# Kernel tuning notes

Hardware: AMD Instinct MI355X
Metric: run time of the kernel (lower is better)

The kernel has to match this reference:

```python
import jax, jax.numpy as jnp
import numpy as np

N, C = 16384, 4096

def setup_inputs() -> dict:
    key = jax.random.key(0)
    k1, k2 = jax.random.split(key)
    preds = jax.random.normal(k1, (N, C), dtype=jnp.float32)
    targets = jax.random.normal(k2, (N, C), dtype=jnp.float32)
    return {"preds": preds, "targets": targets}


def reference(preds, targets):
    # Faithful to My_impute_Loss.forward: the module only RETURNS
    # clusters_pcc_loss + clusters_cossim_loss (per-column stats, axis=1 loop
    # / cosine_similarity(dim=0)); everything else in loss_function is unused.

    # --- per-column Pearson correlation over rows (vectorizes the axis=1 loop) ---
    mu_t = targets.mean(axis=0)                      # [C]
    mu_p = preds.mean(axis=0)                        # [C]
    dt = targets - mu_t                              # [N, C]
    dp = preds - mu_p                                # [N, C]
    sigma_t = jnp.sqrt((dt * dt).mean(axis=0))       # population std per column
    sigma_p = jnp.sqrt((dp * dp).mean(axis=0))
    cov = (dt * dp).mean(axis=0)
    pcc = cov / (sigma_t * sigma_p)
    pcc = jnp.where(jnp.isnan(pcc), jnp.zeros_like(pcc), pcc)  # NaN -> 0, so nanmean == mean
    clusters_pcc_loss = 1.0 - pcc.mean()

    # --- per-column cosine similarity (F.cosine_similarity(dim=0), eps=1e-8) ---
    eps = 1e-8
    norm_p = jnp.maximum(jnp.sqrt((preds * preds).sum(axis=0)), eps)
    norm_t = jnp.maximum(jnp.sqrt((targets * targets).sum(axis=0)), eps)
    cos = (preds * targets).sum(axis=0) / (norm_p * norm_t)
    clusters_cossim_loss = 1.0 - cos.mean()

    return clusters_pcc_loss + clusters_cossim_loss
```

## Files before the change

### kernel.cpp

```cpp
#include <hip/hip_runtime.h>
#include <math.h>

#define NROWS 16384
#define NCOLS 4096
#define RPC   128
#define NCHUNK (NROWS / RPC)

__global__ __launch_bounds__(1024, 8) void stats_partial_kernel(
    const float* __restrict__ preds,
    const float* __restrict__ targets,
    float* __restrict__ partial)
{
    const int col = threadIdx.x * 4;
    const size_t r0 = (size_t)blockIdx.x * RPC;

    const float* __restrict__ pp = preds   + r0 * NCOLS + col;
    const float* __restrict__ tp = targets + r0 * NCOLS + col;

    float4 sp  = {0.f, 0.f, 0.f, 0.f};
    float4 st  = {0.f, 0.f, 0.f, 0.f};
    float4 spp = {0.f, 0.f, 0.f, 0.f};
    float4 stt = {0.f, 0.f, 0.f, 0.f};
    float4 spt = {0.f, 0.f, 0.f, 0.f};

    #pragma unroll 4
    for (int r = 0; r < RPC; ++r) {
        float4 p = *(const float4*)pp;
        float4 t = *(const float4*)tp;
        sp.x  += p.x;        sp.y  += p.y;        sp.z  += p.z;        sp.w  += p.w;
        st.x  += t.x;        st.y  += t.y;        st.z  += t.z;        st.w  += t.w;
        spp.x += p.x * p.x;  spp.y += p.y * p.y;  spp.z += p.z * p.z;  spp.w += p.w * p.w;
        stt.x += t.x * t.x;  stt.y += t.y * t.y;  stt.z += t.z * t.z;  stt.w += t.w * t.w;
        spt.x += p.x * t.x;  spt.y += p.y * t.y;  spt.z += p.z * t.z;  spt.w += p.w * t.w;
        pp += NCOLS;
        tp += NCOLS;
    }

    float* base = partial + ((size_t)blockIdx.x * 5) * NCOLS + col;
    *(float4*)(base + 0 * NCOLS) = sp;
    *(float4*)(base + 1 * NCOLS) = st;
    *(float4*)(base + 2 * NCOLS) = spp;
    *(float4*)(base + 3 * NCOLS) = stt;
    *(float4*)(base + 4 * NCOLS) = spt;
}

__global__ __launch_bounds__(256) void reduce_cols_kernel(
    const float* __restrict__ partial,
    float* __restrict__ out)
{
    const int ci  = threadIdx.x & 15;
    const int gi  = threadIdx.x >> 4;
    const int col = blockIdx.x * 16 + ci;

    float s[5] = {0.f, 0.f, 0.f, 0.f, 0.f};
    #pragma unroll
    for (int gy = gi; gy < NCHUNK; gy += 16) {
        const float* base = partial + ((size_t)gy * 5) * NCOLS + col;
        #pragma unroll
        for (int k = 0; k < 5; ++k) s[k] += base[k * NCOLS];
    }

    __shared__ float red[256][5];
    #pragma unroll
    for (int k = 0; k < 5; ++k) red[threadIdx.x][k] = s[k];
    __syncthreads();

    __shared__ float colval[16];
    if (threadIdx.x < 16) {
        float t[5] = {0.f, 0.f, 0.f, 0.f, 0.f};
        for (int g = 0; g < 16; ++g) {
            #pragma unroll
            for (int k = 0; k < 5; ++k) t[k] += red[threadIdx.x + 16 * g][k];
        }
        const float invN = 1.0f / (float)NROWS;
        float mu_p = t[0] * invN;
        float mu_t = t[1] * invN;
        float var_p = fmaxf(t[2] * invN - mu_p * mu_p, 0.f);
        float var_t = fmaxf(t[3] * invN - mu_t * mu_t, 0.f);
        float cov   = t[4] * invN - mu_p * mu_t;

        float denom = sqrtf(var_p * var_t);
        float pcc = (denom > 0.f) ? (cov / denom) : 0.f;

        float np_ = fmaxf(sqrtf(t[2]), 1e-8f);
        float nt_ = fmaxf(sqrtf(t[3]), 1e-8f);
        float cs  = t[4] / (np_ * nt_);

        colval[threadIdx.x] = pcc + cs;
    }
    __syncthreads();

    if (threadIdx.x == 0) {
        float b = 0.f;
        #pragma unroll
        for (int i = 0; i < 16; ++i) b += colval[i];
        float contrib = 2.0f / 256.0f - b / (float)NCOLS;
        atomicAdd(out, contrib);
    }
}

extern "C" void kernel_launch(void* const* d_in, const int* in_sizes, int n_in,
                              void* d_out, int out_size, void* d_ws, size_t ws_size,
                              hipStream_t stream) {
    const float* preds   = (const float*)d_in[0];
    const float* targets = (const float*)d_in[1];
    float* out = (float*)d_out;
    float* partial = (float*)d_ws;

    hipMemsetAsync(d_out, 0, sizeof(float), stream);

    stats_partial_kernel<<<NCHUNK, 1024, 0, stream>>>(preds, targets, partial);
    reduce_cols_kernel<<<NCOLS / 16, 256, 0, stream>>>(partial, out);
}
```

Before: 130.5 us.

## Split column range across two blocks and zero output inside kernel

The first pass now uses a 2D grid that splits the 4096 columns into two halves, so each thread handles two columns with float2 loads instead of four with float4. This doubles the block count from 128 to 256 so more of the GPU's compute units are occupied. The output scalar is now zeroed by one thread of the first kernel, which removes the separate memset launch. In exchange each load is narrower and per-thread memory-level parallelism is lower, though the unroll is raised to partly make up for it.

```diff
diff --git a/kernel.cpp b/kernel.cpp
--- a/kernel.cpp
+++ b/kernel.cpp
@@ -5,43 +5,48 @@
 #define NCOLS 4096
 #define RPC   128
 #define NCHUNK (NROWS / RPC)
+#define HALF  (NCOLS / 2)
 
 __global__ __launch_bounds__(1024, 8) void stats_partial_kernel(
     const float* __restrict__ preds,
     const float* __restrict__ targets,
-    float* __restrict__ partial)
+    float* __restrict__ partial,
+    float* __restrict__ out)
 {
-    const int col = threadIdx.x * 4;
-    const size_t r0 = (size_t)blockIdx.x * RPC;
+    if (blockIdx.x == 0 && blockIdx.y == 0 && threadIdx.x == 0)
+        out[0] = 0.0f;
+
+    const int col   = blockIdx.x * HALF + threadIdx.x * 2;
+    const size_t r0 = (size_t)blockIdx.y * RPC;
 
     const float* __restrict__ pp = preds   + r0 * NCOLS + col;
     const float* __restrict__ tp = targets + r0 * NCOLS + col;
 
-    float4 sp  = {0.f, 0.f, 0.f, 0.f};
-    float4 st  = {0.f, 0.f, 0.f, 0.f};
-    float4 spp = {0.f, 0.f, 0.f, 0.f};
-    float4 stt = {0.f, 0.f, 0.f, 0.f};
-    float4 spt = {0.f, 0.f, 0.f, 0.f};
+    float2 sp  = {0.f, 0.f};
+    float2 st  = {0.f, 0.f};
+    float2 spp = {0.f, 0.f};
+    float2 stt = {0.f, 0.f};
+    float2 spt = {0.f, 0.f};
 
-    #pragma unroll 4
+    #pragma unroll 8
     for (int r = 0; r < RPC; ++r) {
-        float4 p = *(const float4*)pp;
-        float4 t = *(const float4*)tp;
-        sp.x  += p.x;        sp.y  += p.y;        sp.z  += p.z;        sp.w  += p.w;
-        st.x  += t.x;        st.y  += t.y;        st.z  += t.z;        st.w  += t.w;
-        spp.x += p.x * p.x;  spp.y += p.y * p.y;  spp.z += p.z * p.z;  spp.w += p.w * p.w;
-        stt.x += t.x * t.x;  stt.y += t.y * t.y;  stt.z += t.z * t.z;  stt.w += t.w * t.w;
-        spt.x += p.x * t.x;  spt.y += p.y * t.y;  spt.z += p.z * t.z;  spt.w += p.w * t.w;
+        float2 p = *(const float2*)pp;
+        float2 t = *(const float2*)tp;
+        sp.x  += p.x;        sp.y  += p.y;
+        st.x  += t.x;        st.y  += t.y;
+        spp.x += p.x * p.x;  spp.y += p.y * p.y;
+        stt.x += t.x * t.x;  stt.y += t.y * t.y;
+        spt.x += p.x * t.x;  spt.y += p.y * t.y;
         pp += NCOLS;
         tp += NCOLS;
     }
 
-    float* base = partial + ((size_t)blockIdx.x * 5) * NCOLS + col;
-    *(float4*)(base + 0 * NCOLS) = sp;
-    *(float4*)(base + 1 * NCOLS) = st;
-    *(float4*)(base + 2 * NCOLS) = spp;
-    *(float4*)(base + 3 * NCOLS) = stt;
-    *(float4*)(base + 4 * NCOLS) = spt;
+    float* base = partial + ((size_t)blockIdx.y * 5) * NCOLS + col;
+    *(float2*)(base + 0 * NCOLS) = sp;
+    *(float2*)(base + 1 * NCOLS) = st;
+    *(float2*)(base + 2 * NCOLS) = spp;
+    *(float2*)(base + 3 * NCOLS) = stt;
+    *(float2*)(base + 4 * NCOLS) = spt;
 }
 
 __global__ __launch_bounds__(256) void reduce_cols_kernel(
@@ -107,8 +112,7 @@
     float* out = (float*)d_out;
     float* partial = (float*)d_ws;
 
-    hipMemsetAsync(d_out, 0, sizeof(float), stream);
-
-    stats_partial_kernel<<<NCHUNK, 1024, 0, stream>>>(preds, targets, partial);
+    dim3 grid1(2, NCHUNK);
+    stats_partial_kernel<<<grid1, 1024, 0, stream>>>(preds, targets, partial, out);
     reduce_cols_kernel<<<NCOLS / 16, 256, 0, stream>>>(partial, out);
 }
```

Measured after the change: 106.0 us. 18.8% less time.
